# Performance work log

Hardware: AMD Instinct MI355X
Metric: run time of the kernel (lower is better)

## Reference

```python
import jax, jax.numpy as jnp
import numpy as np

B, S, D, H = 4, 2048, 1024, 16
DK = D // H

def setup_inputs() -> dict:
    key = jax.random.key(0)
    ks = jax.random.split(key, 7)
    f = lambda k, shape: jax.random.normal(k, shape, dtype=jnp.float32)
    return {
        "query": f(ks[0], (B, S, D)),
        "key":   f(ks[1], (B, S, D)),
        "value": f(ks[2], (B, S, D)),
        "w_q": f(ks[3], (D, D)) * (D ** -0.5),
        "w_k": f(ks[4], (D, D)) * (D ** -0.5),
        "w_v": f(ks[5], (D, D)) * (D ** -0.5),
        "w_o": f(ks[6], (D, D)) * (D ** -0.5),
    }

def reference(query, key, value, w_q, w_k, w_v, w_o):
    # Linear layers: y = x @ W^T (torch nn.Linear convention), bias=False
    def split_heads(x):  # [B,S,D] -> [B,H,S,DK]
        return x.reshape(B, S, H, DK).transpose(0, 2, 1, 3)
    Q = split_heads(query @ w_q.T)
    K = split_heads(key @ w_k.T)
    V = split_heads(value @ w_v.T)
    scale = jnp.float32(1.0 / np.sqrt(DK))
    scores = jnp.einsum('bhqd,bhkd->bhqk', Q, K) * scale  # [B,H,Sq,Sk]
    attn = jax.nn.softmax(scores, axis=-1)
    out = jnp.einsum('bhqk,bhkd->bhqd', attn, V)  # [B,H,Sq,DK]
    out = out.transpose(0, 2, 1, 3).reshape(B, S, D)
    return out @ w_o.T
```

## Files before the change

### kernel.cpp

```cpp
#include <hip/hip_runtime.h>
#include <stdint.h>

#define NB 4
#define NS 2048
#define ND 1024
#define NH 16
#define NDK 64
#define NM (NB*NS)

typedef __attribute__((ext_vector_type(8))) short short8;
typedef __attribute__((ext_vector_type(8))) unsigned short ushort8v;
typedef __attribute__((ext_vector_type(4))) float f32x4;
typedef __attribute__((ext_vector_type(16))) float f32x16;

__device__ __forceinline__ unsigned short f2bf(float f) {
  union { float f; uint32_t u; } v; v.f = f;
  uint32_t u = v.u;
  return (unsigned short)((u + 0x7FFFu + ((u >> 16) & 1u)) >> 16);
}

__device__ __forceinline__ uint32_t cvtpk(float lo, float hi) {
  uint32_t r;
  asm("v_cvt_pk_bf16_f32 %0, %1, %2" : "=v"(r) : "v"(lo), "v"(hi));
  return r;
}

__device__ __forceinline__ void gload16(const void* g, void* l) {
  __builtin_amdgcn_global_load_lds(
      (const __attribute__((address_space(1))) void*)g,
      (__attribute__((address_space(3))) void*)l, 16, 0, 0);
}

__device__ __forceinline__ int xcd_swz(int flat, int nwg) {
  return (flat & 7) * (nwg >> 3) + (flat >> 3);
}

__global__ void convert_weights(
    const float* __restrict__ w0, const float* __restrict__ w1,
    const float* __restrict__ w2, const float* __restrict__ w3,
    unsigned short* __restrict__ ow0, unsigned short* __restrict__ ow1,
    unsigned short* __restrict__ ow2, unsigned short* __restrict__ ow3)
{
  size_t e = ((size_t)blockIdx.x * 256 + threadIdx.x) * 8;
  int which = (int)(e >> 20);
  size_t i = e & ((1u << 20) - 1);
  const float* ws[4] = {w0, w1, w2, w3};
  unsigned short* wd[4] = {ow0, ow1, ow2, ow3};
  const float* src = ws[which];
  unsigned short* dst = wd[which];
  f32x4 a = *(const f32x4*)(src + i);
  f32x4 b = *(const f32x4*)(src + i + 4);
  ushort8v h;
  h[0]=f2bf(a.x); h[1]=f2bf(a.y); h[2]=f2bf(a.z); h[3]=f2bf(a.w);
  h[4]=f2bf(b.x); h[5]=f2bf(b.y); h[6]=f2bf(b.z); h[7]=f2bf(b.w);
  *(ushort8v*)(dst + i) = h;
}

template<int OUT, int PRESCALE>
__device__ __forceinline__ void gemm_a32_core(
    const float* __restrict__ X,
    const unsigned short* __restrict__ Wt,
    void* __restrict__ Cout,
    char* lds, int m0, int n0)
{
  const int K = ND, N = ND;
  const int SZB = 49152;
  const int NT = K / 32;
  const int tid = threadIdx.x;
  const int lane = tid & 63, wid = tid >> 6;
  const int l15 = lane & 15, lg = lane >> 4;
  const int wr = wid >> 2, wc = wid & 3;
  const float QSC = 0.125f * 1.44269504088896f;

  const float* Asrc[4];
  int dofA[4];
#pragma unroll
  for (int l = 0; l < 4; ++l) {
    int cidx = l*512 + tid;
    int r = cidx >> 3;
    int c = (cidx & 7) ^ (r & 7);
    Asrc[l] = X + (size_t)(m0 + r)*K + c*4;
    dofA[l] = cidx * 16;
  }
  const unsigned short* Bsrc[2];
  int dofB[2];
#pragma unroll
  for (int l = 0; l < 2; ++l) {
    int cidx = l*512 + tid;
    int r = cidx >> 2;
    int c = (cidx & 3) ^ ((r >> 1) & 3);
    Bsrc[l] = Wt + (size_t)(n0 + r)*K + c*8;
    dofB[l] = cidx * 16;
  }

  f32x4 acc[8][4] = {};

#define STAGEQ(t, buf)                                                         \
  {                                                                            \
    char* d_ = lds + (buf)*SZB;                                                \
    _Pragma("unroll") for (int l = 0; l < 4; ++l)                              \
      gload16(Asrc[l] + (t)*32, d_ + dofA[l]);                                 \
    _Pragma("unroll") for (int l = 0; l < 2; ++l)                              \
      gload16(Bsrc[l] + (t)*32, d_ + 32768 + dofB[l]);                         \
  }

  STAGEQ(0, 0)
  STAGEQ(1, 1)
  asm volatile("s_waitcnt vmcnt(6)" ::: "memory");
  __builtin_amdgcn_s_barrier();

  int b0 = 0;
  for (int t = 0; t < NT; ++t) {
    if (t + 2 < NT) {
      int nb = b0 + 2; if (nb >= 3) nb -= 3;
      STAGEQ(t + 2, nb)
    }
    const char* Ab = lds + b0*SZB;
    const unsigned short* Bb = (const unsigned short*)(lds + b0*SZB + 32768);

    short8 bfr[4];
#pragma unroll
    for (int nn = 0; nn < 4; ++nn) {
      int row = wc*64 + nn*16 + l15;
      bfr[nn] = *(const short8*)(Bb + row*32 + (lg ^ ((row >> 1) & 3))*8);
    }
#pragma unroll
    for (int mh = 0; mh < 2; ++mh) {
      short8 af[4];
#pragma unroll
      for (int mm = 0; mm < 4; ++mm) {
        int row = wr*128 + mh*64 + mm*16 + l15;
        const char* Ar = Ab + row*128;
        int c0 = (2*lg) ^ (row & 7), c1 = (2*lg + 1) ^ (row & 7);
        f32x4 a0 = *(const f32x4*)(Ar + c0*16);
        f32x4 a1 = *(const f32x4*)(Ar + c1*16);
        union { uint32_t u[4]; short8 s; } f;
        f.u[0] = cvtpk(a0.x, a0.y); f.u[1] = cvtpk(a0.z, a0.w);
        f.u[2] = cvtpk(a1.x, a1.y); f.u[3] = cvtpk(a1.z, a1.w);
        af[mm] = f.s;
      }
      __builtin_amdgcn_s_setprio(1);
#pragma unroll
      for (int mm = 0; mm < 4; ++mm)
#pragma unroll
        for (int nn = 0; nn < 4; ++nn)
          acc[mh*4+mm][nn] = __builtin_amdgcn_mfma_f32_16x16x32_bf16(
              af[mm], bfr[nn], acc[mh*4+mm][nn], 0, 0, 0);
      __builtin_amdgcn_s_setprio(0);
    }

    if (t + 2 < NT) {
      asm volatile("s_waitcnt vmcnt(6)" ::: "memory");
      __builtin_amdgcn_s_barrier();
    } else if (t + 1 < NT) {
      asm volatile("s_waitcnt vmcnt(0)" ::: "memory");
      __builtin_amdgcn_s_barrier();
    }
    b0 = (b0 + 1 == 3) ? 0 : b0 + 1;
  }
#undef STAGEQ

#pragma unroll
  for (int m = 0; m < 8; ++m)
#pragma unroll
    for (int n = 0; n < 4; ++n)
#pragma unroll
      for (int i = 0; i < 4; ++i) {
        int row = m0 + wr*128 + m*16 + lg*4 + i;
        int col = n0 + wc*64 + n*16 + l15;
        float val = PRESCALE ? acc[m][n][i] * QSC : acc[m][n][i];
        if (OUT == 1)
          ((unsigned short*)Cout)[(size_t)row * N + col] = f2bf(val);
        else
          ((unsigned short*)Cout)[((size_t)((row >> 11)*1024 + col))*NS + (row & (NS-1))]
              = f2bf(val);
      }
}

__global__ __launch_bounds__(512, 1) void gemm_qkv(
    const float* __restrict__ Xq, const unsigned short* __restrict__ Wq, unsigned short* Qb,
    const float* __restrict__ Xk, const unsigned short* __restrict__ Wk, unsigned short* Kb,
    const float* __restrict__ Xv, const unsigned short* __restrict__ Wv, unsigned short* VbT)
{
  __shared__ char lds[3*49152];
  int flat = (blockIdx.z * 32 + blockIdx.y) * 4 + blockIdx.x;
  int swz = xcd_swz(flat, 384);
  int z = swz >> 7, rem = swz & 127;
  int m0 = (rem >> 2) * 256, n0 = (rem & 3) * 256;
  if (z == 0)      gemm_a32_core<1,1>(Xq, Wq, Qb,  lds, m0, n0);
  else if (z == 1) gemm_a32_core<1,0>(Xk, Wk, Kb,  lds, m0, n0);
  else             gemm_a32_core<2,0>(Xv, Wv, VbT, lds, m0, n0);
}

__global__ __launch_bounds__(512, 2) void gemm_o(
    const unsigned short* __restrict__ A, const unsigned short* __restrict__ Bt, float* C)
{
  __shared__ unsigned short lds[3*8192];
  const int K = ND, N = ND;
  const int SZ = 8192;
  const int NT = K / 32;
  const int tid = threadIdx.x;
  const int lane = tid & 63, wid = tid >> 6;
  const int l15 = lane & 15, lg = lane >> 4;
  const int wr = wid >> 2, wc = wid & 3;
  int flat = blockIdx.y * 8 + blockIdx.x;
  int swz = xcd_swz(flat, 512);
  const int m0 = (swz >> 3) * 128, n0 = (swz & 7) * 128;

  const unsigned short* Asrc;
  const unsigned short* Bsrc;
  int dofA, dofB;
  {
    int r = tid >> 2;
    int c = (tid & 3) ^ ((r >> 1) & 3);
    Asrc = A  + (size_t)(m0 + r)*K + c*8;
    Bsrc = Bt + (size_t)(n0 + r)*K + c*8;
    dofA = tid * 8;
    dofB = 4096 + tid * 8;
  }

  f32x4 acc[4][2] = {};

#define STAGEO(t, buf)                                                         \
  {                                                                            \
    unsigned short* d_ = lds + (buf)*SZ;                                       \
    gload16(Asrc + (t)*32, d_ + dofA);                                         \
    gload16(Bsrc + (t)*32, d_ + dofB);                                         \
  }

  STAGEO(0, 0)
  STAGEO(1, 1)
  asm volatile("s_waitcnt vmcnt(2)" ::: "memory");
  __builtin_amdgcn_s_barrier();

  int b0 = 0;
  for (int t = 0; t < NT; ++t) {
    if (t + 2 < NT) {
      int nb = b0 + 2; if (nb >= 3) nb -= 3;
      STAGEO(t + 2, nb)
    }
    const unsigned short* Abase = lds + b0*SZ;
    const unsigned short* Bbase = lds + b0*SZ + 4096;

    short8 bfr[2];
#pragma unroll
    for (int nn = 0; nn < 2; ++nn) {
      int row = wc*32 + nn*16 + l15;
      bfr[nn] = *(const short8*)(Bbase + row*32 + (lg ^ ((row >> 1) & 3))*8);
    }
    short8 af[4];
#pragma unroll
    for (int mm = 0; mm < 4; ++mm) {
      int row = wr*64 + mm*16 + l15;
      af[mm] = *(const short8*)(Abase + row*32 + (lg ^ ((row >> 1) & 3))*8);
    }
    __builtin_amdgcn_s_setprio(1);
#pragma unroll
    for (int mm = 0; mm < 4; ++mm)
#pragma unroll
      for (int nn = 0; nn < 2; ++nn)
        acc[mm][nn] = __builtin_amdgcn_mfma_f32_16x16x32_bf16(
            af[mm], bfr[nn], acc[mm][nn], 0, 0, 0);
    __builtin_amdgcn_s_setprio(0);

    if (t + 2 < NT) {
      asm volatile("s_waitcnt vmcnt(2)" ::: "memory");
      __builtin_amdgcn_s_barrier();
    } else if (t + 1 < NT) {
      asm volatile("s_waitcnt vmcnt(0)" ::: "memory");
      __builtin_amdgcn_s_barrier();
    }
    b0 = (b0 + 1 == 3) ? 0 : b0 + 1;
  }
#undef STAGEO

#pragma unroll
  for (int m = 0; m < 4; ++m)
#pragma unroll
    for (int n = 0; n < 2; ++n)
#pragma unroll
      for (int i = 0; i < 4; ++i) {
        int row = m0 + wr*64 + m*16 + lg*4 + i;
        int col = n0 + wc*32 + n*16 + l15;
        C[(size_t)row * N + col] = acc[m][n][i];
      }
}

__global__ __launch_bounds__(256, 2) void flash_attn(
    const unsigned short* __restrict__ Qb,
    const unsigned short* __restrict__ Kb,
    const unsigned short* __restrict__ VT,
    unsigned short* __restrict__ O)
{
  __shared__ unsigned short Kt[2][64*64];
  __shared__ unsigned short Vt[2][64*64];
  const int tid = threadIdx.x, lane = tid & 63, wid = tid >> 6;
  const int l31 = lane & 31, hi = lane >> 5;
  int flat = blockIdx.y * 8 + blockIdx.x;
  int swz = xcd_swz(flat, 512);
  const int bh = swz >> 3, b = bh >> 4, h = bh & 15;
  const int q0 = (swz & 7) * 256 + wid * 64;

  const unsigned short* Kp[2]; const unsigned short* Vp[2]; int dofs[2];
#pragma unroll
  for (int p = 0; p < 2; ++p) {
    int slot = tid + p*256;
    int g = slot >> 6, r = slot & 63;
    Kp[p] = Kb + ((size_t)(b*NS + r))*ND + h*64 + g*8;
    Vp[p] = VT + ((size_t)(bh*64 + r))*NS + g*8;
    dofs[p] = slot * 8;
  }

  short8 qf[2][4];
#pragma unroll
  for (int qs = 0; qs < 2; ++qs)
#pragma unroll
    for (int ks = 0; ks < 4; ++ks)
      qf[qs][ks] = *(const short8*)(Qb + (size_t)(b*NS + q0 + qs*32 + l31)*ND + h*64 + ks*16 + hi*8);

  f32x16 oacc[2][2] = {};
  float lsum[2] = {0.f, 0.f};

#pragma unroll
  for (int p = 0; p < 2; ++p) {
    gload16(Kp[p], &Kt[0][dofs[p]]);
    gload16(Vp[p], &Vt[0][dofs[p]]);
  }
  __syncthreads();

  for (int t = 0; t < NS/64; ++t) {
    const int cur = t & 1;
    if (t + 1 < NS/64) {
#pragma unroll
      for (int p = 0; p < 2; ++p) {
        gload16(Kp[p] + (size_t)(t+1)*64*ND, &Kt[cur^1][dofs[p]]);
        gload16(Vp[p] + (t+1)*64,            &Vt[cur^1][dofs[p]]);
      }
    }
    const char* Kc = (const char*)Kt[cur];
    const char* Vc = (const char*)Vt[cur];

    short8 pa[2][2][2];
    float rs[2] = {0.f, 0.f};

#pragma unroll
    for (int n = 0; n < 2; ++n) {
      f32x16 st[2] = {};
      const int r = n*32 + l31;
      __builtin_amdgcn_s_setprio(1);
#pragma unroll
      for (int ks = 0; ks < 4; ++ks) {
        short8 kf = *(const short8*)(Kc + (((2*ks + hi) << 10) + r*16));
        st[0] = __builtin_amdgcn_mfma_f32_32x32x16_bf16(kf, qf[0][ks], st[0], 0, 0, 0);
        st[1] = __builtin_amdgcn_mfma_f32_32x32x16_bf16(kf, qf[1][ks], st[1], 0, 0, 0);
      }
      __builtin_amdgcn_s_setprio(0);
#pragma unroll
      for (int qs = 0; qs < 2; ++qs) {
        float lrs = 0.f;
#pragma unroll
        for (int e = 0; e < 16; ++e) {
          float p = __builtin_amdgcn_exp2f(st[qs][e]);
          st[qs][e] = p;
          lrs += p;
        }
        rs[qs] += lrs;
        uint32_t w[4][2];
#pragma unroll
        for (int e = 0; e < 4; ++e) {
          w[e][0] = cvtpk(st[qs][4*e+0], st[qs][4*e+1]);
          w[e][1] = cvtpk(st[qs][4*e+2], st[qs][4*e+3]);
        }
#pragma unroll
        for (int ksl = 0; ksl < 2; ++ksl) {
          uint32_t a0 = w[2*ksl][0], b0 = w[2*ksl+1][0];
          uint32_t a1 = w[2*ksl][1], b1 = w[2*ksl+1][1];
          asm("v_permlane32_swap_b32 %0, %1" : "+v"(a0), "+v"(b0));
          asm("v_permlane32_swap_b32 %0, %1" : "+v"(a1), "+v"(b1));
          union { uint32_t u[4]; short8 s; } f;
          f.u[0] = a0; f.u[1] = a1; f.u[2] = b0; f.u[3] = b1;
          pa[qs][n][ksl] = f.s;
        }
      }
    }
#pragma unroll
    for (int qs = 0; qs < 2; ++qs) {
      rs[qs] += __shfl_xor(rs[qs], 32);
      lsum[qs] += rs[qs];
    }

    __builtin_amdgcn_s_setprio(1);
#pragma unroll
    for (int d = 0; d < 2; ++d) {
      const int dr = d*32 + l31;
#pragma unroll
      for (int n = 0; n < 2; ++n)
#pragma unroll
        for (int ksl = 0; ksl < 2; ++ksl) {
          const int g = n*4 + ksl*2 + hi;
          short8 vf = *(const short8*)(Vc + ((g << 10) + dr*16));
          oacc[0][d] = __builtin_amdgcn_mfma_f32_32x32x16_bf16(pa[0][n][ksl], vf, oacc[0][d], 0, 0, 0);
          oacc[1][d] = __builtin_amdgcn_mfma_f32_32x32x16_bf16(pa[1][n][ksl], vf, oacc[1][d], 0, 0, 0);
        }
    }
    __builtin_amdgcn_s_setprio(0);
    __syncthreads();
  }

#pragma unroll
  for (int qs = 0; qs < 2; ++qs) {
    float linv[16];
#pragma unroll
    for (int r = 0; r < 16; ++r)
      linv[r] = 1.0f / __shfl(lsum[qs], (r & 3) + 8*(r >> 2) + 4*hi);
#pragma unroll
    for (int d = 0; d < 2; ++d)
#pragma unroll
      for (int r = 0; r < 16; ++r) {
        int qrow = q0 + qs*32 + (r & 3) + 8*(r >> 2) + 4*hi;
        O[(size_t)(b*NS + qrow)*ND + h*64 + d*32 + l31] = f2bf(oacc[qs][d][r] * linv[r]);
      }
  }
}

extern "C" void kernel_launch(void* const* d_in, const int* in_sizes, int n_in,
                              void* d_out, int out_size, void* d_ws, size_t ws_size,
                              hipStream_t stream) {
  const float* q  = (const float*)d_in[0];
  const float* k  = (const float*)d_in[1];
  const float* v  = (const float*)d_in[2];
  const float* wq = (const float*)d_in[3];
  const float* wk = (const float*)d_in[4];
  const float* wv = (const float*)d_in[5];
  const float* wo = (const float*)d_in[6];

  unsigned short* Wq = (unsigned short*)d_ws;
  unsigned short* Wk = Wq + (size_t)ND*ND;
  unsigned short* Wv = Wk + (size_t)ND*ND;
  unsigned short* Wo = Wv + (size_t)ND*ND;
  unsigned short* Qb = Wo + (size_t)ND*ND;
  unsigned short* Kb = Qb + (size_t)NM*ND;
  unsigned short* Ob = Kb + (size_t)NM*ND;
  unsigned short* VbT = (unsigned short*)d_out;

  convert_weights<<<2048, 256, 0, stream>>>(wq, wk, wv, wo, Wq, Wk, Wv, Wo);

  gemm_qkv<<<dim3(4, 32, 3), 512, 0, stream>>>(q, Wq, Qb, k, Wk, Kb, v, Wv, VbT);

  flash_attn<<<dim3(8, 64), 256, 0, stream>>>(Qb, Kb, VbT, Ob);

  gemm_o<<<dim3(8, 64), 512, 0, stream>>>(Ob, Wo, (float*)d_out);
}
```

Baseline: 200.1 us.

## Pre-convert activations to bf16 in a separate pass and simplify QKV GEMM

Activations q/k/v are now converted to bf16 in a combined conversion kernel alongside the weights, and the QKV GEMM loads bf16 A tiles directly instead of fp32 tiles with in-loop packing. This cuts LDS footprint and in-loop conversion work, but adds an extra full read of fp32 inputs and a write/read of bf16 copies in global memory. Separately, the flash attention row-sum cross-lane shuffle is moved out of the KV loop to the epilogue.

```diff
diff --git a/kernel.cpp b/kernel.cpp
--- a/kernel.cpp
+++ b/kernel.cpp
@@ -35,19 +35,30 @@
   return (flat & 7) * (nwg >> 3) + (flat >> 3);
 }
 
-__global__ void convert_weights(
+__global__ void convert_all(
+    const float* __restrict__ x0, const float* __restrict__ x1, const float* __restrict__ x2,
     const float* __restrict__ w0, const float* __restrict__ w1,
     const float* __restrict__ w2, const float* __restrict__ w3,
+    unsigned short* __restrict__ ox0, unsigned short* __restrict__ ox1, unsigned short* __restrict__ ox2,
     unsigned short* __restrict__ ow0, unsigned short* __restrict__ ow1,
     unsigned short* __restrict__ ow2, unsigned short* __restrict__ ow3)
 {
-  size_t e = ((size_t)blockIdx.x * 256 + threadIdx.x) * 8;
-  int which = (int)(e >> 20);
-  size_t i = e & ((1u << 20) - 1);
-  const float* ws[4] = {w0, w1, w2, w3};
-  unsigned short* wd[4] = {ow0, ow1, ow2, ow3};
-  const float* src = ws[which];
-  unsigned short* dst = wd[which];
+  const float* src;
+  unsigned short* dst;
+  size_t i;
+  if (blockIdx.y < 3) {
+    src = blockIdx.y == 0 ? x0 : (blockIdx.y == 1 ? x1 : x2);
+    dst = blockIdx.y == 0 ? ox0 : (blockIdx.y == 1 ? ox1 : ox2);
+    i = ((size_t)blockIdx.x * 256 + threadIdx.x) * 8;
+  } else {
+    if (blockIdx.x >= 2048) return;
+    size_t e = ((size_t)blockIdx.x * 256 + threadIdx.x) * 8;
+    int which = (int)(e >> 20);
+    size_t off = e & ((1u << 20) - 1);
+    const float* ws[4] = {w0, w1, w2, w3};
+    unsigned short* wd[4] = {ow0, ow1, ow2, ow3};
+    src = ws[which]; dst = wd[which]; i = off;
+  }
   f32x4 a = *(const f32x4*)(src + i);
   f32x4 b = *(const f32x4*)(src + i + 4);
   ushort8v h;
@@ -57,14 +68,14 @@
 }
 
 template<int OUT, int PRESCALE>
-__device__ __forceinline__ void gemm_a32_core(
-    const float* __restrict__ X,
-    const unsigned short* __restrict__ Wt,
+__device__ __forceinline__ void gemm_bk32_core(
+    const unsigned short* __restrict__ A,
+    const unsigned short* __restrict__ Bt,
     void* __restrict__ Cout,
-    char* lds, int m0, int n0)
+    unsigned short* lds, int m0, int n0)
 {
   const int K = ND, N = ND;
-  const int SZB = 49152;
+  const int ASZ = 8192, SZ = 16384;
   const int NT = K / 32;
   const int tid = threadIdx.x;
   const int lane = tid & 63, wid = tid >> 6;
@@ -72,57 +83,50 @@
   const int wr = wid >> 2, wc = wid & 3;
   const float QSC = 0.125f * 1.44269504088896f;
 
-  const float* Asrc[4];
-  int dofA[4];
-#pragma unroll
-  for (int l = 0; l < 4; ++l) {
-    int cidx = l*512 + tid;
-    int r = cidx >> 3;
-    int c = (cidx & 7) ^ (r & 7);
-    Asrc[l] = X + (size_t)(m0 + r)*K + c*4;
-    dofA[l] = cidx * 16;
-  }
+  const unsigned short* Asrc[2];
   const unsigned short* Bsrc[2];
-  int dofB[2];
+  int dofA[2], dofB[2];
 #pragma unroll
   for (int l = 0; l < 2; ++l) {
     int cidx = l*512 + tid;
     int r = cidx >> 2;
-    int c = (cidx & 3) ^ ((r >> 1) & 3);
-    Bsrc[l] = Wt + (size_t)(n0 + r)*K + c*8;
-    dofB[l] = cidx * 16;
+    int ch = (cidx & 3) ^ ((r >> 1) & 3);
+    Asrc[l] = A + (size_t)(m0 + r)*K + ch*8;
+    dofA[l] = cidx * 8;
+    Bsrc[l] = Bt + (size_t)(n0 + r)*K + ch*8;
+    dofB[l] = cidx * 8;
   }
 
   f32x4 acc[8][4] = {};
 
-#define STAGEQ(t, buf)                                                         \
+#define STAGE32(t, buf)                                                        \
   {                                                                            \
-    char* d_ = lds + (buf)*SZB;                                                \
-    _Pragma("unroll") for (int l = 0; l < 4; ++l)                              \
+    unsigned short* d_ = lds + (buf)*SZ;                                       \
+    _Pragma("unroll") for (int l = 0; l < 2; ++l)                              \
       gload16(Asrc[l] + (t)*32, d_ + dofA[l]);                                 \
     _Pragma("unroll") for (int l = 0; l < 2; ++l)                              \
-      gload16(Bsrc[l] + (t)*32, d_ + 32768 + dofB[l]);                         \
-  }
-
-  STAGEQ(0, 0)
-  STAGEQ(1, 1)
-  asm volatile("s_waitcnt vmcnt(6)" ::: "memory");
+      gload16(Bsrc[l] + (t)*32, d_ + ASZ + dofB[l]);                           \
+  }
+
+  STAGE32(0, 0)
+  STAGE32(1, 1)
+  asm volatile("s_waitcnt vmcnt(4)" ::: "memory");
   __builtin_amdgcn_s_barrier();
 
   int b0 = 0;
   for (int t = 0; t < NT; ++t) {
     if (t + 2 < NT) {
       int nb = b0 + 2; if (nb >= 3) nb -= 3;
-      STAGEQ(t + 2, nb)
-    }
-    const char* Ab = lds + b0*SZB;
-    const unsigned short* Bb = (const unsigned short*)(lds + b0*SZB + 32768);
+      STAGE32(t + 2, nb)
+    }
+    const unsigned short* Abase = lds + b0*SZ;
+    const unsigned short* Bbase = lds + b0*SZ + ASZ;
 
     short8 bfr[4];
 #pragma unroll
     for (int nn = 0; nn < 4; ++nn) {
       int row = wc*64 + nn*16 + l15;
-      bfr[nn] = *(const short8*)(Bb + row*32 + (lg ^ ((row >> 1) & 3))*8);
+      bfr[nn] = *(const short8*)(Bbase + row*32 + (lg ^ ((row >> 1) & 3))*8);
     }
 #pragma unroll
     for (int mh = 0; mh < 2; ++mh) {
@@ -130,14 +134,7 @@
 #pragma unroll
       for (int mm = 0; mm < 4; ++mm) {
         int row = wr*128 + mh*64 + mm*16 + l15;
-        const char* Ar = Ab + row*128;
-        int c0 = (2*lg) ^ (row & 7), c1 = (2*lg + 1) ^ (row & 7);
-        f32x4 a0 = *(const f32x4*)(Ar + c0*16);
-        f32x4 a1 = *(const f32x4*)(Ar + c1*16);
-        union { uint32_t u[4]; short8 s; } f;
-        f.u[0] = cvtpk(a0.x, a0.y); f.u[1] = cvtpk(a0.z, a0.w);
-        f.u[2] = cvtpk(a1.x, a1.y); f.u[3] = cvtpk(a1.z, a1.w);
-        af[mm] = f.s;
+        af[mm] = *(const short8*)(Abase + row*32 + (lg ^ ((row >> 1) & 3))*8);
       }
       __builtin_amdgcn_s_setprio(1);
 #pragma unroll
@@ -150,7 +147,7 @@
     }
 
     if (t + 2 < NT) {
-      asm volatile("s_waitcnt vmcnt(6)" ::: "memory");
+      asm volatile("s_waitcnt vmcnt(4)" ::: "memory");
       __builtin_amdgcn_s_barrier();
     } else if (t + 1 < NT) {
       asm volatile("s_waitcnt vmcnt(0)" ::: "memory");
@@ -158,7 +155,7 @@
     }
     b0 = (b0 + 1 == 3) ? 0 : b0 + 1;
   }
-#undef STAGEQ
+#undef STAGE32
 
 #pragma unroll
   for (int m = 0; m < 8; ++m)
@@ -178,18 +175,18 @@
 }
 
 __global__ __launch_bounds__(512, 1) void gemm_qkv(
-    const float* __restrict__ Xq, const unsigned short* __restrict__ Wq, unsigned short* Qb,
-    const float* __restrict__ Xk, const unsigned short* __restrict__ Wk, unsigned short* Kb,
-    const float* __restrict__ Xv, const unsigned short* __restrict__ Wv, unsigned short* VbT)
+    const unsigned short* __restrict__ Xq, const unsigned short* __restrict__ Wq, unsigned short* Qb,
+    const unsigned short* __restrict__ Xk, const unsigned short* __restrict__ Wk, unsigned short* Kb,
+    const unsigned short* __restrict__ Xv, const unsigned short* __restrict__ Wv, unsigned short* VbT)
 {
-  __shared__ char lds[3*49152];
+  __shared__ unsigned short lds[3*16384];
   int flat = (blockIdx.z * 32 + blockIdx.y) * 4 + blockIdx.x;
   int swz = xcd_swz(flat, 384);
   int z = swz >> 7, rem = swz & 127;
   int m0 = (rem >> 2) * 256, n0 = (rem & 3) * 256;
-  if (z == 0)      gemm_a32_core<1,1>(Xq, Wq, Qb,  lds, m0, n0);
-  else if (z == 1) gemm_a32_core<1,0>(Xk, Wk, Kb,  lds, m0, n0);
-  else             gemm_a32_core<2,0>(Xv, Wv, VbT, lds, m0, n0);
+  if (z == 0)      gemm_bk32_core<1,1>(Xq, Wq, Qb,  lds, m0, n0);
+  else if (z == 1) gemm_bk32_core<1,0>(Xk, Wk, Kb,  lds, m0, n0);
+  else             gemm_bk32_core<2,0>(Xv, Wv, VbT, lds, m0, n0);
 }
 
 __global__ __launch_bounds__(512, 2) void gemm_o(
@@ -341,7 +338,6 @@
     const char* Vc = (const char*)Vt[cur];
 
     short8 pa[2][2][2];
-    float rs[2] = {0.f, 0.f};
 
 #pragma unroll
     for (int n = 0; n < 2; ++n) {
@@ -364,7 +360,7 @@
           st[qs][e] = p;
           lrs += p;
         }
-        rs[qs] += lrs;
+        lsum[qs] += lrs;
         uint32_t w[4][2];
 #pragma unroll
         for (int e = 0; e < 4; ++e) {
@@ -383,11 +379,6 @@
         }
       }
     }
-#pragma unroll
-    for (int qs = 0; qs < 2; ++qs) {
-      rs[qs] += __shfl_xor(rs[qs], 32);
-      lsum[qs] += rs[qs];
-    }
 
     __builtin_amdgcn_s_setprio(1);
 #pragma unroll
@@ -409,6 +400,7 @@
 
 #pragma unroll
   for (int qs = 0; qs < 2; ++qs) {
+    lsum[qs] += __shfl_xor(lsum[qs], 32);
     float linv[16];
 #pragma unroll
     for (int r = 0; r < 16; ++r)
@@ -438,14 +430,18 @@
   unsigned short* Wk = Wq + (size_t)ND*ND;
   unsigned short* Wv = Wk + (size_t)ND*ND;
   unsigned short* Wo = Wv + (size_t)ND*ND;
-  unsigned short* Qb = Wo + (size_t)ND*ND;
+  unsigned short* Xq = Wo + (size_t)ND*ND;
+  unsigned short* Xk = Xq + (size_t)NM*ND;
+  unsigned short* Xv = Xk + (size_t)NM*ND;
+  unsigned short* Qb = Xv + (size_t)NM*ND;
   unsigned short* Kb = Qb + (size_t)NM*ND;
-  unsigned short* Ob = Kb + (size_t)NM*ND;
   unsigned short* VbT = (unsigned short*)d_out;
-
-  convert_weights<<<2048, 256, 0, stream>>>(wq, wk, wv, wo, Wq, Wk, Wv, Wo);
-
-  gemm_qkv<<<dim3(4, 32, 3), 512, 0, stream>>>(q, Wq, Qb, k, Wk, Kb, v, Wv, VbT);
+  unsigned short* Ob  = Xq;
+
+  convert_all<<<dim3(NM*ND/(256*8), 4), 256, 0, stream>>>(
+      q, k, v, wq, wk, wv, wo, Xq, Xk, Xv, Wq, Wk, Wv, Wo);
+
+  gemm_qkv<<<dim3(4, 32, 3), 512, 0, stream>>>(Xq, Wq, Qb, Xk, Wk, Kb, Xv, Wv, VbT);
 
   flash_attn<<<dim3(8, 64), 256, 0, stream>>>(Qb, Kb, VbT, Ob);
 
```

Result: no change. 201.8 us (+0.8%).
